# Kernel tuning notes

Hardware: AMD Instinct MI355X
Metric: run time of the kernel (lower is better)

Reference implementation:

```python
import jax, jax.numpy as jnp
import numpy as np

D_MODEL = 1024
NUM_HEADS = 16
HEAD_DIM = D_MODEL // NUM_HEADS  # 64
B, S = 2, 2048


def setup_inputs() -> dict:
    key = jax.random.key(0)
    k1, k2, k3, k4, k5 = jax.random.split(key, 5)
    scale = 1.0 / np.sqrt(D_MODEL)
    return {
        "x": jax.random.normal(k1, (B, S, D_MODEL), dtype=jnp.float32),
        "Wq": jax.random.normal(k2, (D_MODEL, D_MODEL), dtype=jnp.float32) * scale,
        "bq": jax.random.normal(k3, (D_MODEL,), dtype=jnp.float32) * 0.02,
        "Wv": jax.random.normal(k4, (D_MODEL, D_MODEL), dtype=jnp.float32) * scale,
        "bv": jax.random.normal(k5, (D_MODEL,), dtype=jnp.float32) * 0.02,
    }


def reference(x, Wq, bq, Wv, bv):
    b, s, _ = x.shape
    d, n = HEAD_DIM, NUM_HEADS
    # nn.Linear: y = x @ W.T + b
    Q = x @ Wq.T + bq
    # NOTE (faithful to source bug): K uses the VALUE projection, key weights unused.
    KV = x @ Wv.T + bv
    # einops 'B S (d n) -> B S d n' -> 'B n S d'  (head index n is fast-varying)
    Qh = Q.reshape(b, s, d, n).transpose(0, 3, 1, 2)   # [B, n, S, d]
    Kt = KV.reshape(b, s, d, n).transpose(0, 3, 2, 1)  # [B, n, d, S]
    Vh = KV.reshape(b, s, d, n).transpose(0, 3, 1, 2)  # [B, n, S, d]
    scores = jnp.matmul(Qh, Kt) / jnp.sqrt(jnp.float32(d))  # [B, n, S, S]
    attn = jnp.matmul(jax.nn.softmax(scores, axis=-1), Vh)  # [B, n, S, d]
    # 'B n S d -> B S (n d)'
    out = attn.transpose(0, 2, 1, 3).reshape(b, s, n * d)
    return out
```

## Files before the change

### kernel.cpp

```cpp
#include <hip/hip_runtime.h>
#include <hip/hip_bf16.h>
#include <math.h>


typedef __bf16 bf16x8 __attribute__((ext_vector_type(8)));
typedef float  f32x4  __attribute__((ext_vector_type(4)));
typedef short  s16x4  __attribute__((ext_vector_type(4)));
typedef unsigned short ushort_t;
typedef unsigned short us8 __attribute__((ext_vector_type(8)));

#define QSCALE 0.1803368801111204f

__device__ __forceinline__ unsigned short f2bf(float f) {
  unsigned int u = __builtin_bit_cast(unsigned int, f);
  u += 0x7fffu + ((u >> 16) & 1u);
  return (unsigned short)(u >> 16);
}

__device__ __forceinline__ unsigned int pk2(float a, float b) {
  unsigned int ua = __builtin_bit_cast(unsigned int, a) + 0x8000u;
  unsigned int ub = __builtin_bit_cast(unsigned int, b) + 0x8000u;
  return (ua >> 16) | (ub & 0xffff0000u);
}

__device__ __forceinline__ unsigned int cvtpk(float lo, float hi) {
  unsigned int r;
  asm("v_cvt_pk_bf16_f32 %0, %1, %2" : "=v"(r) : "v"(lo), "v"(hi));
  return r;
}

__device__ __forceinline__ void gl_lds16(const void* g, void* l) {
  __builtin_amdgcn_global_load_lds(
      (const __attribute__((address_space(1))) unsigned int*)g,
      (__attribute__((address_space(3))) unsigned int*)l, 16, 0, 0);
}

__device__ __forceinline__ f32x4 mfma_k32(bf16x8 a, bf16x8 b, f32x4 c) {
  return __builtin_amdgcn_mfma_f32_16x16x32_bf16(a, b, c, 0, 0, 0);
}
__device__ __forceinline__ f32x4 mfma_k16(s16x4 a, s16x4 b, f32x4 c) {
  return __builtin_amdgcn_mfma_f32_16x16x16bf16_1k(a, b, c, 0, 0, 0);
}

__global__ __launch_bounds__(256) void cvt3_kernel(const float4* __restrict__ x,
                                                   const float4* __restrict__ wq,
                                                   const float4* __restrict__ wv,
                                                   ushort4* __restrict__ dst) {
  const int i = blockIdx.x * 256 + threadIdx.x;
  const float4 v = (i < 1048576) ? x[i]
                 : (i < 1310720) ? wq[i - 1048576]
                                 : wv[i - 1310720];
  ushort4 o;
  o.x = f2bf(v.x); o.y = f2bf(v.y); o.z = f2bf(v.z); o.w = f2bf(v.w);
  dst[i] = o;
}

__global__ __launch_bounds__(256) void proj_kernel(
    const ushort_t* __restrict__ X,
    const ushort_t* __restrict__ Wqm,
    const ushort_t* __restrict__ Wvm,
    const float*    __restrict__ bq,
    const float*    __restrict__ bv,
    ushort_t* __restrict__ Qh,
    ushort_t* __restrict__ KVh,
    ushort_t* __restrict__ KVt)
{
  __shared__ __align__(16) unsigned char lds[32768];
  const int tid = threadIdx.x;
  const int w  = tid >> 6;
  const int l  = tid & 63;
  const int lq = l >> 4;
  const int ll = l & 15;
  const bool isQ = (blockIdx.z == 0);
  const ushort_t* Wmat = isQ ? Wqm : Wvm;
  const float*    bias = isQ ? bq  : bv;
  const int m0 = blockIdx.x * 128;
  const int by = blockIdx.y;
  const int wm = (w & 1) * 64;
  const int wn = (w >> 1) * 64;

  f32x4 acc[4][4] = {};

  for (int k0 = 0; k0 < 1024; k0 += 64) {
    __syncthreads();
#pragma unroll
    for (int t = 0; t < 4; ++t) {
      const int seg = w * 4 + t;
      const int r = seg * 8 + (l >> 3);
      const int cd = (l & 7) ^ (r & 7);
      const int cg = by * 128 + r;
      const int wrow = ((cg & 63) << 4) | (cg >> 6);
      gl_lds16(X    + (size_t)(m0 + r) * 1024 + k0 + cd * 8, lds + seg * 1024);
      gl_lds16(Wmat + (size_t)wrow * 1024 + k0 + cd * 8, lds + 16384 + seg * 1024);
    }
    __syncthreads();
#pragma unroll
    for (int kb = 0; kb < 2; ++kb) {
      const int kc = kb * 4 + lq;
      bf16x8 af[4], bfr[4];
#pragma unroll
      for (int mi = 0; mi < 4; ++mi) {
        const int m = wm + mi * 16 + ll;
        af[mi] = *(const bf16x8*)(lds + m * 128 + ((kc ^ (m & 7)) * 16));
      }
#pragma unroll
      for (int ni = 0; ni < 4; ++ni) {
        const int n = wn + ni * 16 + ll;
        bfr[ni] = *(const bf16x8*)(lds + 16384 + n * 128 + ((kc ^ (n & 7)) * 16));
      }
#pragma unroll
      for (int mi = 0; mi < 4; ++mi)
#pragma unroll
        for (int ni = 0; ni < 4; ++ni)
          acc[mi][ni] = mfma_k32(af[mi], bfr[ni], acc[mi][ni]);
    }
  }

  const int hl = wn >> 6;
  const int hh = by * 2 + hl;
  const int b  = m0 >> 11;
  const int sbase = m0 & 2047;

  if (isQ) {
#pragma unroll
    for (int ni = 0; ni < 4; ++ni) {
      const int ii = ni * 16 + ll;
      const float bb = bias[(ii << 4) | hh];
#pragma unroll
      for (int mi = 0; mi < 4; ++mi)
#pragma unroll
        for (int r = 0; r < 4; ++r) {
          const int s = sbase + wm + mi * 16 + lq * 4 + r;
          const float v = acc[mi][ni][r] + bb;
          Qh[(((size_t)(b * 16 + hh)) * 2048 + s) * 64 + ii] = f2bf(v * QSCALE);
        }
    }
  } else {
    __syncthreads();
#pragma unroll
    for (int ni = 0; ni < 4; ++ni) {
      const int ii = ni * 16 + ll;
      const float bb = bias[(ii << 4) | hh];
#pragma unroll
      for (int mi = 0; mi < 4; ++mi) {
        const float v0 = acc[mi][ni][0] + bb;
        const float v1 = acc[mi][ni][1] + bb;
        const float v2 = acc[mi][ni][2] + bb;
        const float v3 = acc[mi][ni][3] + bb;
        const unsigned int u01 = pk2(v0, v1);
        const unsigned int u23 = pk2(v2, v3);
        const int sl = wm + mi * 16 + lq * 4;
        const size_t kb0 = (((size_t)(b * 16 + hh)) * 2048 + sbase + sl) * 64 + ii;
        KVh[kb0]       = (ushort_t)(u01 & 0xffffu);
        KVh[kb0 + 64]  = (ushort_t)(u01 >> 16);
        KVh[kb0 + 128] = (ushort_t)(u23 & 0xffffu);
        KVh[kb0 + 192] = (ushort_t)(u23 >> 16);
        const int g = (wm >> 2) + mi * 4 + lq;
        const int pc = (g >> 1) ^ ll;
        *(uint2*)(lds + hl * 16384 + ii * 256 + pc * 16 + (g & 1) * 8) =
            make_uint2(u01, u23);
      }
    }
    __syncthreads();
    const int row = tid >> 1;
    const int hl2 = row >> 6, ii2 = row & 63;
    const int cbase = (tid & 1) * 8;
    ushort_t* dst = KVt + (((size_t)(b * 16 + by * 2 + hl2)) * 64 + ii2) * 2048 + sbase;
#pragma unroll
    for (int cc = 0; cc < 8; ++cc) {
      const int c = cbase + cc;
      const int pc = c ^ (ii2 & 15);
      const us8 v = *(const us8*)(lds + hl2 * 16384 + ii2 * 256 + pc * 16);
      *(us8*)(dst + c * 8) = v;
    }
  }
}

__global__ __launch_bounds__(128, 2) void attn_kernel(
    const ushort_t* __restrict__ Qh,
    const ushort_t* __restrict__ KVh,
    const ushort_t* __restrict__ KVt,
    float* __restrict__ out)
{
  __shared__ __align__(16) unsigned char sm[32768];
  const int tid = threadIdx.x;
  const int w  = tid >> 6;
  const int l  = tid & 63;
  const int quad = l >> 4;
  const int ll = l & 15;
  const int bid = blockIdx.x;
  const int bh = ((bid & 7) << 2) | (bid >> 8);
  const int qt = (bid >> 3) & 31;
  const int b = bh >> 4, h = bh & 15;
  const int qw = qt * 64 + w * 32;
  const ushort_t* Qhead  = Qh  + (size_t)bh * (2048 * 64);
  const ushort_t* Khead  = KVh + (size_t)bh * (2048 * 64);
  const ushort_t* Vthead = KVt + (size_t)bh * (64 * 2048);

  bf16x8 qf[2][2];
#pragma unroll
  for (int c = 0; c < 2; ++c)
#pragma unroll
    for (int kb = 0; kb < 2; ++kb)
      qf[c][kb] = *(const bf16x8*)(Qhead + (size_t)(qw + c * 16 + ll) * 64 +
                                   kb * 32 + quad * 8);

  f32x4 O[2][4] = {};
  float l_run[2] = {0.f, 0.f};

#pragma unroll
  for (int t = 0; t < 8; ++t) {
    const int seg = w * 8 + t;
    const int r = seg * 8 + (l >> 3);
    const int cd = (l & 7) ^ (r & 7);
    gl_lds16(Khead + (size_t)r * 64 + cd * 8, sm + seg * 1024);
  }

  for (int kt = 0; kt < 16; ++kt) {
    const int sk0 = kt * 128;
    asm volatile("s_waitcnt lgkmcnt(0)" ::: "memory");
    __builtin_amdgcn_sched_barrier(0);
    __builtin_amdgcn_s_barrier();
    __builtin_amdgcn_sched_barrier(0);
#pragma unroll
    for (int t = 0; t < 8; ++t) {
      const int seg = w * 8 + t;
      const int d = seg * 4 + (l >> 4);
      const int c8 = (l & 15) ^ (d & 15);
      gl_lds16(Vthead + (size_t)d * 2048 + sk0 + c8 * 8, sm + 16384 + seg * 1024);
    }
    asm volatile("s_waitcnt vmcnt(8)" ::: "memory");
    __builtin_amdgcn_sched_barrier(0);
    __builtin_amdgcn_s_barrier();
    __builtin_amdgcn_sched_barrier(0);

    f32x4 Sa[2][8] = {};
#pragma unroll
    for (int kb = 0; kb < 2; ++kb) {
      const int kc = kb * 4 + quad;
#pragma unroll
      for (int ni = 0; ni < 8; ++ni) {
        const int n = ni * 16 + ll;
        const bf16x8 ak = *(const bf16x8*)(sm + n * 128 + ((kc ^ (n & 7)) * 16));
        Sa[0][ni] = mfma_k32(ak, qf[0][kb], Sa[0][ni]);
        Sa[1][ni] = mfma_k32(ak, qf[1][kb], Sa[1][ni]);
      }
    }

    asm volatile("s_waitcnt lgkmcnt(0)" ::: "memory");
    __builtin_amdgcn_sched_barrier(0);
    __builtin_amdgcn_s_barrier();
    __builtin_amdgcn_sched_barrier(0);
    if (kt < 15) {
      const int sk1 = sk0 + 128;
#pragma unroll
      for (int t = 0; t < 8; ++t) {
        const int seg = w * 8 + t;
        const int r = seg * 8 + (l >> 3);
        const int cd = (l & 7) ^ (r & 7);
        gl_lds16(Khead + (size_t)(sk1 + r) * 64 + cd * 8, sm + seg * 1024);
      }
    }

    s16x4 pk[2][8];
#pragma unroll
    for (int c = 0; c < 2; ++c) {
      float ps = 0.f;
#pragma unroll
      for (int ni = 0; ni < 8; ++ni) {
        const float p0 = __builtin_amdgcn_exp2f(Sa[c][ni][0]);
        const float p1 = __builtin_amdgcn_exp2f(Sa[c][ni][1]);
        const float p2 = __builtin_amdgcn_exp2f(Sa[c][ni][2]);
        const float p3 = __builtin_amdgcn_exp2f(Sa[c][ni][3]);
        ps += (p0 + p1) + (p2 + p3);
        const uint2 uu = make_uint2(cvtpk(p0, p1), cvtpk(p2, p3));
        pk[c][ni] = __builtin_bit_cast(s16x4, uu);
      }
      l_run[c] += ps;
    }

    if (kt < 15) { asm volatile("s_waitcnt vmcnt(8)" ::: "memory"); }
    else         { asm volatile("s_waitcnt vmcnt(0)" ::: "memory"); }
    __builtin_amdgcn_sched_barrier(0);
    __builtin_amdgcn_s_barrier();
    __builtin_amdgcn_sched_barrier(0);

#pragma unroll
    for (int ni = 0; ni < 8; ++ni) {
      const int cb = 2 * ni + (quad >> 1);
#pragma unroll
      for (int no = 0; no < 4; ++no) {
        const int row = no * 16 + ll;
        const s16x4 bv = *(const s16x4*)(sm + 16384 + row * 256 +
                                         ((cb ^ ll) * 16) + (quad & 1) * 8);
        O[0][no] = mfma_k16(pk[0][ni], bv, O[0][no]);
        O[1][no] = mfma_k16(pk[1][ni], bv, O[1][no]);
      }
    }
  }

#pragma unroll
  for (int c = 0; c < 2; ++c) {
    float s = l_run[c];
    s += __shfl_xor(s, 16);
    s += __shfl_xor(s, 32);
    const float inv = 1.f / s;
    float invr[4];
#pragma unroll
    for (int r = 0; r < 4; ++r)
      invr[r] = __shfl(inv, (l & 48) + ((l & 48) >> 2) + r);
    float* op = out + ((size_t)(b * 2048) + qw + c * 16) * 1024 + h * 64;
#pragma unroll
    for (int no = 0; no < 4; ++no)
#pragma unroll
      for (int r = 0; r < 4; ++r) {
        const int q = quad * 4 + r;
        op[(size_t)q * 1024 + no * 16 + ll] = O[c][no][r] * invr[r];
      }
  }
}

extern "C" void kernel_launch(void* const* d_in, const int* in_sizes, int n_in,
                              void* d_out, int out_size, void* d_ws, size_t ws_size,
                              hipStream_t stream) {
  const float* x  = (const float*)d_in[0];
  const float* Wq = (const float*)d_in[1];
  const float* bq = (const float*)d_in[2];
  const float* Wv = (const float*)d_in[3];
  const float* bv = (const float*)d_in[4];
  float* out = (float*)d_out;
  char* ws = (char*)d_ws;

  ushort_t* xbf  = (ushort_t*)(ws);
  ushort_t* wqbf = (ushort_t*)(ws + 8388608);
  ushort_t* wvbf = (ushort_t*)(ws + 10485760);
  ushort_t* Qh   = (ushort_t*)(ws + 12582912);
  ushort_t* KVh  = (ushort_t*)(ws + 20971520);
  ushort_t* KVt  = (ushort_t*)(ws + 29360128);

  cvt3_kernel<<<6144, 256, 0, stream>>>((const float4*)x, (const float4*)Wq,
                                        (const float4*)Wv, (ushort4*)xbf);
  proj_kernel<<<dim3(32, 8, 2), 256, 0, stream>>>(xbf, wqbf, wvbf, bq, bv,
                                                  Qh, KVh, KVt);
  attn_kernel<<<1024, 128, 0, stream>>>(Qh, KVh, KVt, out);
}
```

Baseline: 154.8 us.

## Split attention keys across waves and shrink projection tiles to one head

The attention kernel now has both waves share all 64 queries while each wave handles half of every 128-key tile. Partial O and row sums are reduced through LDS at the end, which removes two block barriers per key tile. Separately, the projection kernel switches to 128x64 tiles covering a single head per block, doubling the grid to 1024 blocks for better occupancy. The cost is more register pressure from larger per-wave accumulators, an extra LDS reduction, and less weight reuse per projection tile.

```diff
diff --git a/kernel.cpp b/kernel.cpp
--- a/kernel.cpp
+++ b/kernel.cpp
@@ -65,7 +65,7 @@
     ushort_t* __restrict__ KVh,
     ushort_t* __restrict__ KVt)
 {
-  __shared__ __align__(16) unsigned char lds[32768];
+  __shared__ __align__(16) unsigned char lds[24576];
   const int tid = threadIdx.x;
   const int w  = tid >> 6;
   const int l  = tid & 63;
@@ -76,10 +76,9 @@
   const float*    bias = isQ ? bq  : bv;
   const int m0 = blockIdx.x * 128;
   const int by = blockIdx.y;
-  const int wm = (w & 1) * 64;
-  const int wn = (w >> 1) * 64;
-
-  f32x4 acc[4][4] = {};
+  const int wm = w * 32;
+
+  f32x4 acc[2][4] = {};
 
   for (int k0 = 0; k0 < 1024; k0 += 64) {
     __syncthreads();
@@ -88,36 +87,40 @@
       const int seg = w * 4 + t;
       const int r = seg * 8 + (l >> 3);
       const int cd = (l & 7) ^ (r & 7);
-      const int cg = by * 128 + r;
-      const int wrow = ((cg & 63) << 4) | (cg >> 6);
-      gl_lds16(X    + (size_t)(m0 + r) * 1024 + k0 + cd * 8, lds + seg * 1024);
+      gl_lds16(X + (size_t)(m0 + r) * 1024 + k0 + cd * 8, lds + seg * 1024);
+    }
+#pragma unroll
+    for (int t = 0; t < 2; ++t) {
+      const int seg = w * 2 + t;
+      const int r = seg * 8 + (l >> 3);
+      const int cd = (l & 7) ^ (r & 7);
+      const int wrow = (r << 4) | by;
       gl_lds16(Wmat + (size_t)wrow * 1024 + k0 + cd * 8, lds + 16384 + seg * 1024);
     }
     __syncthreads();
 #pragma unroll
     for (int kb = 0; kb < 2; ++kb) {
       const int kc = kb * 4 + lq;
-      bf16x8 af[4], bfr[4];
-#pragma unroll
-      for (int mi = 0; mi < 4; ++mi) {
+      bf16x8 af[2], bfr[4];
+#pragma unroll
+      for (int mi = 0; mi < 2; ++mi) {
         const int m = wm + mi * 16 + ll;
         af[mi] = *(const bf16x8*)(lds + m * 128 + ((kc ^ (m & 7)) * 16));
       }
 #pragma unroll
       for (int ni = 0; ni < 4; ++ni) {
-        const int n = wn + ni * 16 + ll;
+        const int n = ni * 16 + ll;
         bfr[ni] = *(const bf16x8*)(lds + 16384 + n * 128 + ((kc ^ (n & 7)) * 16));
       }
 #pragma unroll
-      for (int mi = 0; mi < 4; ++mi)
+      for (int mi = 0; mi < 2; ++mi)
 #pragma unroll
         for (int ni = 0; ni < 4; ++ni)
           acc[mi][ni] = mfma_k32(af[mi], bfr[ni], acc[mi][ni]);
     }
   }
 
-  const int hl = wn >> 6;
-  const int hh = by * 2 + hl;
+  const int hh = by;
   const int b  = m0 >> 11;
   const int sbase = m0 & 2047;
 
@@ -127,7 +130,7 @@
       const int ii = ni * 16 + ll;
       const float bb = bias[(ii << 4) | hh];
 #pragma unroll
-      for (int mi = 0; mi < 4; ++mi)
+      for (int mi = 0; mi < 2; ++mi)
 #pragma unroll
         for (int r = 0; r < 4; ++r) {
           const int s = sbase + wm + mi * 16 + lq * 4 + r;
@@ -142,7 +145,7 @@
       const int ii = ni * 16 + ll;
       const float bb = bias[(ii << 4) | hh];
 #pragma unroll
-      for (int mi = 0; mi < 4; ++mi) {
+      for (int mi = 0; mi < 2; ++mi) {
         const float v0 = acc[mi][ni][0] + bb;
         const float v1 = acc[mi][ni][1] + bb;
         const float v2 = acc[mi][ni][2] + bb;
@@ -155,22 +158,21 @@
         KVh[kb0 + 64]  = (ushort_t)(u01 >> 16);
         KVh[kb0 + 128] = (ushort_t)(u23 & 0xffffu);
         KVh[kb0 + 192] = (ushort_t)(u23 >> 16);
-        const int g = (wm >> 2) + mi * 4 + lq;
+        const int g = w * 8 + mi * 4 + lq;
         const int pc = (g >> 1) ^ ll;
-        *(uint2*)(lds + hl * 16384 + ii * 256 + pc * 16 + (g & 1) * 8) =
+        *(uint2*)(lds + ii * 256 + pc * 16 + (g & 1) * 8) =
             make_uint2(u01, u23);
       }
     }
     __syncthreads();
-    const int row = tid >> 1;
-    const int hl2 = row >> 6, ii2 = row & 63;
-    const int cbase = (tid & 1) * 8;
-    ushort_t* dst = KVt + (((size_t)(b * 16 + by * 2 + hl2)) * 64 + ii2) * 2048 + sbase;
-#pragma unroll
-    for (int cc = 0; cc < 8; ++cc) {
+    const int ii2 = tid >> 2;
+    const int cbase = (tid & 3) * 4;
+    ushort_t* dst = KVt + (((size_t)(b * 16 + by)) * 64 + ii2) * 2048 + sbase;
+#pragma unroll
+    for (int cc = 0; cc < 4; ++cc) {
       const int c = cbase + cc;
       const int pc = c ^ (ii2 & 15);
-      const us8 v = *(const us8*)(lds + hl2 * 16384 + ii2 * 256 + pc * 16);
+      const us8 v = *(const us8*)(lds + ii2 * 256 + pc * 16);
       *(us8*)(dst + c * 8) = v;
     }
   }
@@ -192,22 +194,23 @@
   const int bh = ((bid & 7) << 2) | (bid >> 8);
   const int qt = (bid >> 3) & 31;
   const int b = bh >> 4, h = bh & 15;
-  const int qw = qt * 64 + w * 32;
+  const int qw = qt * 64;
   const ushort_t* Qhead  = Qh  + (size_t)bh * (2048 * 64);
   const ushort_t* Khead  = KVh + (size_t)bh * (2048 * 64);
   const ushort_t* Vthead = KVt + (size_t)bh * (64 * 2048);
 
-  bf16x8 qf[2][2];
-#pragma unroll
-  for (int c = 0; c < 2; ++c)
+  bf16x8 qf[4][2];
+#pragma unroll
+  for (int c = 0; c < 4; ++c)
 #pragma unroll
     for (int kb = 0; kb < 2; ++kb)
       qf[c][kb] = *(const bf16x8*)(Qhead + (size_t)(qw + c * 16 + ll) * 64 +
                                    kb * 32 + quad * 8);
 
-  f32x4 O[2][4] = {};
-  float l_run[2] = {0.f, 0.f};
-
+  f32x4 O[4][4] = {};
+  float l_run[4] = {0.f, 0.f, 0.f, 0.f};
+
+  __builtin_amdgcn_sched_barrier(0);
 #pragma unroll
   for (int t = 0; t < 8; ++t) {
     const int seg = w * 8 + t;
@@ -231,25 +234,23 @@
     }
     asm volatile("s_waitcnt vmcnt(8)" ::: "memory");
     __builtin_amdgcn_sched_barrier(0);
-    __builtin_amdgcn_s_barrier();
-    __builtin_amdgcn_sched_barrier(0);
-
-    f32x4 Sa[2][8] = {};
+
+    f32x4 Sa[4][4] = {};
 #pragma unroll
     for (int kb = 0; kb < 2; ++kb) {
       const int kc = kb * 4 + quad;
 #pragma unroll
-      for (int ni = 0; ni < 8; ++ni) {
-        const int n = ni * 16 + ll;
+      for (int ni = 0; ni < 4; ++ni) {
+        const int n = w * 64 + ni * 16 + ll;
         const bf16x8 ak = *(const bf16x8*)(sm + n * 128 + ((kc ^ (n & 7)) * 16));
         Sa[0][ni] = mfma_k32(ak, qf[0][kb], Sa[0][ni]);
         Sa[1][ni] = mfma_k32(ak, qf[1][kb], Sa[1][ni]);
+        Sa[2][ni] = mfma_k32(ak, qf[2][kb], Sa[2][ni]);
+        Sa[3][ni] = mfma_k32(ak, qf[3][kb], Sa[3][ni]);
       }
     }
 
     asm volatile("s_waitcnt lgkmcnt(0)" ::: "memory");
-    __builtin_amdgcn_sched_barrier(0);
-    __builtin_amdgcn_s_barrier();
     __builtin_amdgcn_sched_barrier(0);
     if (kt < 15) {
       const int sk1 = sk0 + 128;
@@ -262,12 +263,12 @@
       }
     }
 
-    s16x4 pk[2][8];
-#pragma unroll
-    for (int c = 0; c < 2; ++c) {
+    s16x4 pk[4][4];
+#pragma unroll
+    for (int c = 0; c < 4; ++c) {
       float ps = 0.f;
 #pragma unroll
-      for (int ni = 0; ni < 8; ++ni) {
+      for (int ni = 0; ni < 4; ++ni) {
         const float p0 = __builtin_amdgcn_exp2f(Sa[c][ni][0]);
         const float p1 = __builtin_amdgcn_exp2f(Sa[c][ni][1]);
         const float p2 = __builtin_amdgcn_exp2f(Sa[c][ni][2]);
@@ -286,8 +287,8 @@
     __builtin_amdgcn_sched_barrier(0);
 
 #pragma unroll
-    for (int ni = 0; ni < 8; ++ni) {
-      const int cb = 2 * ni + (quad >> 1);
+    for (int ni = 0; ni < 4; ++ni) {
+      const int cb = w * 8 + 2 * ni + (quad >> 1);
 #pragma unroll
       for (int no = 0; no < 4; ++no) {
         const int row = no * 16 + ll;
@@ -295,13 +296,35 @@
                                          ((cb ^ ll) * 16) + (quad & 1) * 8);
         O[0][no] = mfma_k16(pk[0][ni], bv, O[0][no]);
         O[1][no] = mfma_k16(pk[1][ni], bv, O[1][no]);
-      }
-    }
-  }
-
-#pragma unroll
-  for (int c = 0; c < 2; ++c) {
-    float s = l_run[c];
+        O[2][no] = mfma_k16(pk[2][ni], bv, O[2][no]);
+        O[3][no] = mfma_k16(pk[3][ni], bv, O[3][no]);
+      }
+    }
+  }
+
+  asm volatile("s_waitcnt lgkmcnt(0)" ::: "memory");
+  __builtin_amdgcn_sched_barrier(0);
+  __builtin_amdgcn_s_barrier();
+  __builtin_amdgcn_sched_barrier(0);
+#pragma unroll
+  for (int j = 0; j < 2; ++j) {
+    const int c = (1 - w) * 2 + j;
+#pragma unroll
+    for (int no = 0; no < 4; ++no)
+      *(f32x4*)(sm + c * 4096 + no * 1024 + l * 16) = O[c][no];
+    *(float*)(sm + 16384 + c * 256 + l * 4) = l_run[c];
+  }
+  asm volatile("s_waitcnt lgkmcnt(0)" ::: "memory");
+  __builtin_amdgcn_sched_barrier(0);
+  __builtin_amdgcn_s_barrier();
+  __builtin_amdgcn_sched_barrier(0);
+#pragma unroll
+  for (int j = 0; j < 2; ++j) {
+    const int c = 2 * w + j;
+#pragma unroll
+    for (int no = 0; no < 4; ++no)
+      O[c][no] += *(const f32x4*)(sm + c * 4096 + no * 1024 + l * 16);
+    float s = l_run[c] + *(const float*)(sm + 16384 + c * 256 + l * 4);
     s += __shfl_xor(s, 16);
     s += __shfl_xor(s, 32);
     const float inv = 1.f / s;
@@ -340,7 +363,7 @@
 
   cvt3_kernel<<<6144, 256, 0, stream>>>((const float4*)x, (const float4*)Wq,
                                         (const float4*)Wv, (ushort4*)xbf);
-  proj_kernel<<<dim3(32, 8, 2), 256, 0, stream>>>(xbf, wqbf, wvbf, bq, bv,
-                                                  Qh, KVh, KVt);
+  proj_kernel<<<dim3(32, 16, 2), 256, 0, stream>>>(xbf, wqbf, wvbf, bq, bv,
+                                                   Qh, KVh, KVt);
   attn_kernel<<<1024, 128, 0, stream>>>(Qh, KVh, KVt, out);
 }
```

New measurement: 182.7 us. 18.0% more time.
